# Kernel tuning notes

Hardware: AMD Instinct MI355X
Metric: run time of the kernel (lower is better)

Reference implementation:

```python
import jax, jax.numpy as jnp
import numpy as np


def setup_inputs() -> dict:
    key = jax.random.key(0)
    k1, k2, k3 = jax.random.split(key, 3)
    bs, chart_len, H = 256, 1024, 256
    num_steps, start_index = 512, 512
    chart = jax.random.normal(k1, (bs, chart_len, 2 * H), dtype=jnp.float32)
    operations = jax.random.randint(k2, (num_steps, bs, 2), 0, start_index, dtype=jnp.int64)
    U = jax.random.normal(k3, (5 * H, 2 * H), dtype=jnp.float32) * 0.05
    b = jnp.zeros((5 * H,), dtype=jnp.float32)
    return {"chart": chart, "operations": operations, "start_index": start_index, "U": U, "b": b}


def reference(chart, operations, start_index, U, b):
    H = U.shape[0] // 5
    bs = chart.shape[0]
    batch_idx = jnp.arange(bs)
    num_steps = operations.shape[0]

    def step_fn(ch, xs):
        step, ops = xs
        left = ch[batch_idx, ops[:, 0]]   # [bs, 2H]
        right = ch[batch_idx, ops[:, 1]]  # [bs, 2H]
        ccL, ccR = left[:, :H], right[:, :H]
        hh = jnp.concatenate([left[:, H:], right[:, H:]], axis=-1)  # [bs, 2H]
        preact = hh @ U.T + b  # [bs, 5H]
        i = jax.nn.sigmoid(preact[:, :H])
        fL = jax.nn.sigmoid(preact[:, H:2 * H])
        fR = jax.nn.sigmoid(preact[:, 2 * H:3 * H])
        o = jax.nn.sigmoid(preact[:, 3 * H:4 * H])
        u = jnp.tanh(preact[:, 4 * H:5 * H])
        c = fL * ccL + fR * ccR + i * u
        h = o * jnp.tanh(c)
        ch = ch.at[:, start_index + step, :].set(jnp.concatenate([c, h], axis=-1))
        return ch, None

    chart, _ = jax.lax.scan(step_fn, chart, (jnp.arange(num_steps), operations))
    return chart
```

## Files before the change

### kernel.cpp

```cpp
#include <hip/hip_runtime.h>
#include <hip/hip_bf16.h>

#define H_     256
#define TWOH_  512
#define CL_    1024
#define BS_    256
#define START_ 512

typedef float  f32x16   __attribute__((ext_vector_type(16)));
typedef short  short8_t __attribute__((ext_vector_type(8)));
typedef short  short4_t __attribute__((ext_vector_type(4)));
typedef __bf16 bf16x8   __attribute__((ext_vector_type(8)));

static __device__ __forceinline__ unsigned short f2bf(float x) {
  __hip_bfloat16 h = __float2bfloat16(x);
  return __builtin_bit_cast(unsigned short, h);
}

static __device__ __forceinline__ void gload16(const void* g, void* l) {
  __builtin_amdgcn_global_load_lds(
      (const __attribute__((address_space(1))) void*)g,
      (__attribute__((address_space(3))) void*)l, 16, 0, 0);
}

#define SCHED0() __builtin_amdgcn_sched_barrier(0)

__global__ void uconv_kernel(const float* __restrict__ U,
                             unsigned short* __restrict__ ub) {
  int tid = blockIdx.x * 256 + threadIdx.x;
  if (tid >= 1280 * 512) return;
  int n = tid >> 9, k = tid & 511;
  int g = n >> 8, j = n & 255;
  int jc = j >> 6, c = (g << 6) + (j & 63);
  ub[((jc * 320 + c) << 9) + k] = f2bf(U[tid]);
}

__global__ void hbcopy_kernel(const float4* __restrict__ chart4,
                              float4* __restrict__ out4,
                              unsigned short* __restrict__ hb) {
  const long long total = 16777216LL;
  long long tid = (long long)blockIdx.x * blockDim.x + threadIdx.x;
  for (long long e = tid; e < total; e += (long long)gridDim.x * blockDim.x) {
    long long i   = e >> 16;
    long long rem = e & 65535;
    long long off = (i << 17) + rem;
    float4 f = chart4[off];
    out4[off] = f;
    int col4 = (int)(rem & 127);
    if (col4 >= 64) {
      long long pos = rem >> 7;
      short4_t v;
      v[0] = (short)f2bf(f.x); v[1] = (short)f2bf(f.y);
      v[2] = (short)f2bf(f.z); v[3] = (short)f2bf(f.w);
      *(short4_t*)(hb + ((i * 512 + pos) * 256 + (long long)(col4 - 64) * 4)) = v;
    }
  }
}

__global__ void copy_kernel(const float4* __restrict__ src,
                            float4* __restrict__ dst) {
  long long tid = (long long)blockIdx.x * blockDim.x + threadIdx.x;
  const long long total = 16777216LL;
  for (long long e = tid; e < total; e += (long long)gridDim.x * blockDim.x) {
    long long i   = e >> 16;
    long long rem = e & 65535;
    long long off = (i << 17) + rem;
    dst[off] = src[off];
  }
}

__global__ __launch_bounds__(256, 2) void chart10_kernel(
    const float* __restrict__ chart,
    const int* __restrict__ ops,
    const unsigned short* __restrict__ ub,
    const unsigned short* __restrict__ hb,
    const float* __restrict__ bias,
    float* __restrict__ out)
{
  __shared__ unsigned short As[2][128 * 32];
  __shared__ unsigned short Bs[2][320 * 32];
  __shared__ int opsl[256];

  const int tid = threadIdx.x, lane = tid & 63, wid = tid >> 6;
  const int l31 = lane & 31, lhi = lane >> 5;
  const int wm = wid >> 1, wn = wid & 1;

  const int bx = blockIdx.x;
  const int g  = (bx & 7) * 512 + (bx >> 3);
  const int s  = g >> 3, mg = (g >> 2) & 1, jc = g & 3;

  opsl[tid] = ops[((size_t)s * BS_ + mg * 128) * 2 + tid];
  __syncthreads();

  const int asrc = (tid & 3) ^ (((tid >> 2) ^ (tid >> 4)) & 3);
  int opL256[2], opR256[2];
  const unsigned short* hbA[2];
  #pragma unroll
  for (int p = 0; p < 2; ++p) {
    int rl = p * 64 + (tid >> 2);
    opL256[p] = opsl[2 * rl] * 256;
    opR256[p] = opsl[2 * rl + 1] * 256;
    hbA[p] = hb + ((size_t)(mg * 128 + rl) * 512) * 256 + asrc * 8;
  }
  const unsigned short* ubB[5];
  #pragma unroll
  for (int p = 0; p < 5; ++p) {
    ubB[p] = ub + (((size_t)(jc * 320 + p * 64 + (tid >> 2))) << 9) + asrc * 8;
  }

  f32x16 acc0[5], acc1[5];
  #pragma unroll
  for (int gg = 0; gg < 5; ++gg)
    #pragma unroll
    for (int q = 0; q < 16; ++q) { acc0[gg][q] = 0.f; acc1[gg][q] = 0.f; }

#define STAGE(BUF, KT) do {                                                     \
    const int koff_ = ((KT) < 8) ? (KT) * 32 : (KT) * 32 - 256;                 \
    _Pragma("unroll")                                                           \
    for (int p = 0; p < 2; ++p) {                                               \
      gload16(hbA[p] + (((KT) < 8) ? opL256[p] : opR256[p]) + koff_,            \
              &As[BUF][(p * 256 + tid) * 8]);                                   \
    }                                                                           \
    _Pragma("unroll")                                                           \
    for (int p = 0; p < 5; ++p) {                                               \
      gload16(ubB[p] + (KT) * 32, &Bs[BUF][(p * 256 + tid) * 8]);               \
    }                                                                           \
  } while (0)

  const int sw   = (l31 ^ (l31 >> 2)) & 3;
  const int aro0 = (wm * 64 + l31) * 32;
  const int aro1 = aro0 + 32 * 32;
  const int bro  = (wn * 32 + l31) * 32;

#define COMPUTE(BUF) do {                                                       \
    _Pragma("unroll")                                                           \
    for (int ks = 0; ks < 2; ++ks) {                                            \
      const int ce = ((ks * 2 + lhi) ^ sw) * 8;                                 \
      bf16x8 a0 = __builtin_bit_cast(bf16x8,                                    \
          *(const short8_t*)&As[BUF][aro0 + ce]);                               \
      bf16x8 a1 = __builtin_bit_cast(bf16x8,                                    \
          *(const short8_t*)&As[BUF][aro1 + ce]);                               \
      _Pragma("unroll")                                                         \
      for (int gg = 0; gg < 5; ++gg) {                                          \
        bf16x8 b = __builtin_bit_cast(bf16x8,                                   \
            *(const short8_t*)&Bs[BUF][bro + gg * 2048 + ce]);                  \
        acc0[gg] = __builtin_amdgcn_mfma_f32_32x32x16_bf16(a0,b,acc0[gg],0,0,0);\
        acc1[gg] = __builtin_amdgcn_mfma_f32_32x32x16_bf16(a1,b,acc1[gg],0,0,0);\
      }                                                                         \
    }                                                                           \
  } while (0)

#define PHASE(BUF, KT, DOSTAGE) do {                                            \
    asm volatile("s_waitcnt vmcnt(7)" ::: "memory");                            \
    __builtin_amdgcn_s_barrier();                                               \
    SCHED0();                                                                   \
    __builtin_amdgcn_s_setprio(1);                                              \
    COMPUTE(BUF);                                                               \
    __builtin_amdgcn_s_setprio(0);                                              \
    SCHED0();                                                                   \
    __builtin_amdgcn_s_barrier();                                               \
    SCHED0();                                                                   \
    if (DOSTAGE) { STAGE(BUF, (KT) + 2); SCHED0(); }                            \
  } while (0)

  STAGE(0, 0); SCHED0();
  STAGE(1, 1); SCHED0();

  #pragma unroll
  for (int kt = 0; kt < 14; kt += 2) {
    PHASE(0, kt,     true);
    PHASE(1, kt + 1, true);
  }
  PHASE(0, 14, false);
  asm volatile("s_waitcnt vmcnt(0)" ::: "memory");
  __builtin_amdgcn_s_barrier();
  SCHED0();
  __builtin_amdgcn_s_setprio(1);
  COMPUTE(1);
  __builtin_amdgcn_s_setprio(0);

#undef PHASE
#undef COMPUTE
#undef STAGE

  const int jlane = jc * 64 + wn * 32 + l31;
  float bg[5];
  #pragma unroll
  for (int gg = 0; gg < 5; ++gg) bg[gg] = bias[gg * H_ + jlane];

#define EPI(ACC, MF) do {                                                       \
    _Pragma("unroll")                                                           \
    for (int q = 0; q < 16; ++q) {                                              \
      const int rl_  = wm * 64 + (MF) * 32 + (q & 3) + 8 * (q >> 2) + 4 * lhi;  \
      const int i_   = mg * 128 + rl_;                                          \
      const int opL_ = opsl[2 * rl_], opR_ = opsl[2 * rl_ + 1];                 \
      const float ccL_ = chart[((size_t)i_ * CL_ + opL_) * TWOH_ + jlane];      \
      const float ccR_ = chart[((size_t)i_ * CL_ + opR_) * TWOH_ + jlane];      \
      float pi_  = (ACC)[0][q] + bg[0];                                         \
      float pfL_ = (ACC)[1][q] + bg[1];                                         \
      float pfR_ = (ACC)[2][q] + bg[2];                                         \
      float po_  = (ACC)[3][q] + bg[3];                                         \
      float pu_  = (ACC)[4][q] + bg[4];                                         \
      float gi_  = 1.f / (1.f + __expf(-pi_));                                  \
      float gfL_ = 1.f / (1.f + __expf(-pfL_));                                 \
      float gfR_ = 1.f / (1.f + __expf(-pfR_));                                 \
      float go_  = 1.f / (1.f + __expf(-po_));                                  \
      float eu_  = __expf(2.f * pu_);                                           \
      float gu_  = 1.f - 2.f / (eu_ + 1.f);                                     \
      float c_   = gfL_ * ccL_ + gfR_ * ccR_ + gi_ * gu_;                       \
      float ec_  = __expf(2.f * c_);                                            \
      float th_  = 1.f - 2.f / (ec_ + 1.f);                                     \
      float h_   = go_ * th_;                                                   \
      float* orow_ = out + ((size_t)i_ * CL_ + START_ + s) * TWOH_;             \
      orow_[jlane]      = c_;                                                   \
      orow_[H_ + jlane] = h_;                                                   \
    }                                                                           \
  } while (0)

  EPI(acc0, 0);
  EPI(acc1, 1);
#undef EPI
}

__global__ __launch_bounds__(256, 2) void chart1_kernel(
    const float* __restrict__ chart,
    const int* __restrict__ ops,
    const float* __restrict__ U,
    const float* __restrict__ bias,
    float* __restrict__ out)
{
  __shared__ unsigned short As[64 * 72];
  __shared__ unsigned short Bs[320 * 72];
  __shared__ int opsl[128];

  const int tid = threadIdx.x, lane = tid & 63, wid = tid >> 6;
  const int wm = wid & 1, wn = wid >> 1;
  const int bx = blockIdx.x, jc = blockIdx.y;
  const int s = bx >> 2, ibase = (bx & 3) * 64, j0 = jc * 64;

  if (tid < 128) opsl[tid] = ops[(s * BS_ + ibase) * 2 + tid];
  __syncthreads();

  const int arow = tid >> 2, aqc = tid & 3;
  const int opL_s = opsl[2 * arow], opR_s = opsl[2 * arow + 1];
  const long long abase_i = (long long)(ibase + arow) * CL_;

  f32x16 acc[5];
  #pragma unroll
  for (int g = 0; g < 5; ++g)
    #pragma unroll
    for (int q = 0; q < 16; ++q) acc[g][q] = 0.0f;

  const int a_off  = (wm * 32 + (lane & 31)) * 72 + 8 * (lane >> 5);
  const int b_off0 = (wn * 32 + (lane & 31)) * 72 + 8 * (lane >> 5);

  for (int kt = 0; kt < 8; ++kt) {
    const int k0 = kt * 64;
    {
      const int op   = (k0 < 256) ? opL_s : opR_s;
      const int col0 = ((k0 < 256) ? 256 + k0 : k0) + aqc * 16;
      const float* src = chart + (abase_i + op) * TWOH_ + col0;
      float4 f0 = *(const float4*)(src + 0);
      float4 f1 = *(const float4*)(src + 4);
      float4 f2 = *(const float4*)(src + 8);
      float4 f3 = *(const float4*)(src + 12);
      short8_t v0, v1;
      v0[0] = (short)f2bf(f0.x); v0[1] = (short)f2bf(f0.y);
      v0[2] = (short)f2bf(f0.z); v0[3] = (short)f2bf(f0.w);
      v0[4] = (short)f2bf(f1.x); v0[5] = (short)f2bf(f1.y);
      v0[6] = (short)f2bf(f1.z); v0[7] = (short)f2bf(f1.w);
      v1[0] = (short)f2bf(f2.x); v1[1] = (short)f2bf(f2.y);
      v1[2] = (short)f2bf(f2.z); v1[3] = (short)f2bf(f2.w);
      v1[4] = (short)f2bf(f3.x); v1[5] = (short)f2bf(f3.y);
      v1[6] = (short)f2bf(f3.z); v1[7] = (short)f2bf(f3.w);
      *(short8_t*)&As[arow * 72 + aqc * 16]     = v0;
      *(short8_t*)&As[arow * 72 + aqc * 16 + 8] = v1;
    }
    #pragma unroll
    for (int cc = 0; cc < 20; ++cc) {
      int chunk = cc * 256 + tid;
      int c  = chunk >> 4;
      int ko = (chunk & 15) * 4;
      int n  = ((c >> 6) << 8) + j0 + (c & 63);
      float4 f = *(const float4*)(U + (long long)n * 512 + k0 + ko);
      short4_t v;
      v[0] = (short)f2bf(f.x); v[1] = (short)f2bf(f.y);
      v[2] = (short)f2bf(f.z); v[3] = (short)f2bf(f.w);
      *(short4_t*)&Bs[c * 72 + ko] = v;
    }
    __syncthreads();

    #pragma unroll
    for (int ks = 0; ks < 4; ++ks) {
      bf16x8 a = __builtin_bit_cast(bf16x8, *(const short8_t*)&As[a_off + ks * 16]);
      #pragma unroll
      for (int g = 0; g < 5; ++g) {
        bf16x8 b = __builtin_bit_cast(bf16x8,
            *(const short8_t*)&Bs[b_off0 + g * 64 * 72 + ks * 16]);
        acc[g] = __builtin_amdgcn_mfma_f32_32x32x16_bf16(a, b, acc[g], 0, 0, 0);
      }
    }
    __syncthreads();
  }

  const int jlane = j0 + wn * 32 + (lane & 31);
  float bg[5];
  #pragma unroll
  for (int g = 0; g < 5; ++g) bg[g] = bias[g * H_ + jlane];

  #pragma unroll
  for (int q = 0; q < 16; ++q) {
    int rl  = wm * 32 + (q & 3) + 8 * (q >> 2) + 4 * (lane >> 5);
    int i   = ibase + rl;
    int opL = opsl[2 * rl], opR = opsl[2 * rl + 1];
    float ccL = chart[((long long)i * CL_ + opL) * TWOH_ + jlane];
    float ccR = chart[((long long)i * CL_ + opR) * TWOH_ + jlane];
    float pi  = acc[0][q] + bg[0];
    float pfL = acc[1][q] + bg[1];
    float pfR = acc[2][q] + bg[2];
    float po  = acc[3][q] + bg[3];
    float pu  = acc[4][q] + bg[4];
    float gi  = 1.f / (1.f + __expf(-pi));
    float gfL = 1.f / (1.f + __expf(-pfL));
    float gfR = 1.f / (1.f + __expf(-pfR));
    float go  = 1.f / (1.f + __expf(-po));
    float eu  = __expf(2.f * pu);
    float gu  = 1.f - 2.f / (eu + 1.f);
    float c   = gfL * ccL + gfR * ccR + gi * gu;
    float ec  = __expf(2.f * c);
    float th  = 1.f - 2.f / (ec + 1.f);
    float h   = go * th;
    float* orow = out + ((long long)i * CL_ + START_ + s) * TWOH_;
    orow[jlane]      = c;
    orow[H_ + jlane] = h;
  }
}

extern "C" void kernel_launch(void* const* d_in, const int* in_sizes, int n_in,
                              void* d_out, int out_size, void* d_ws, size_t ws_size,
                              hipStream_t stream) {
  const float* chart = (const float*)d_in[0];
  const int*   ops   = (const int*)d_in[1];
  const float* U     = (const float*)d_in[3];
  const float* bias  = (const float*)d_in[4];
  float* out = (float*)d_out;

  const size_t HB_OFF   = (size_t)2 << 20;
  const size_t HB_BYTES = (size_t)256 * 512 * 256 * 2;

  if (ws_size >= HB_OFF + HB_BYTES) {
    unsigned short* ub = (unsigned short*)d_ws;
    unsigned short* hb = (unsigned short*)((char*)d_ws + HB_OFF);
    uconv_kernel<<<2560, 256, 0, stream>>>(U, ub);
    hbcopy_kernel<<<4096, 256, 0, stream>>>((const float4*)chart, (float4*)out, hb);
    chart10_kernel<<<4096, 256, 0, stream>>>(chart, ops, ub, hb, bias, out);
  } else {
    copy_kernel<<<4096, 256, 0, stream>>>((const float4*)chart, (float4*)out);
    chart1_kernel<<<dim3(2048, 4), 256, 0, stream>>>(chart, ops, U, bias, out);
  }
}
```

Baseline: 442.4 us.

## Pre-gather bf16 hidden operands into contiguous buffer before GEMM

Adds a kernel that gathers the left/right hidden halves for every step and batch row into a contiguous bf16 matrix, so the main GEMM kernel streams A tiles contiguously instead of gathering through ops indices. The chart copy is now a plain copy rather than fused with bf16 conversion. This trades indirect loads in the GEMM for a large extra materialization pass and requires a much larger workspace, falling back to the old path otherwise.

```diff
diff --git a/kernel.cpp b/kernel.cpp
--- a/kernel.cpp
+++ b/kernel.cpp
@@ -33,6 +33,28 @@
   int g = n >> 8, j = n & 255;
   int jc = j >> 6, c = (g << 6) + (j & 63);
   ub[((jc * 320 + c) << 9) + k] = f2bf(U[tid]);
+}
+
+__global__ void gather_ga_kernel(const float* __restrict__ chart,
+                                 const int* __restrict__ ops,
+                                 unsigned short* __restrict__ ga) {
+  long long t = (long long)blockIdx.x * 256 + threadIdx.x;
+  long long i_s = t >> 6;
+  int c = (int)(t & 63);
+  int k0 = c * 8;
+  int half = (k0 < 256) ? 0 : 1;
+  int koff = (k0 < 256) ? k0 : k0 - 256;
+  int i = (int)(i_s & 255);
+  int op = ops[i_s * 2 + half];
+  const float* src = chart + ((size_t)i * CL_ + op) * TWOH_ + H_ + koff;
+  float4 f0 = *(const float4*)(src);
+  float4 f1 = *(const float4*)(src + 4);
+  short8_t v;
+  v[0] = (short)f2bf(f0.x); v[1] = (short)f2bf(f0.y);
+  v[2] = (short)f2bf(f0.z); v[3] = (short)f2bf(f0.w);
+  v[4] = (short)f2bf(f1.x); v[5] = (short)f2bf(f1.y);
+  v[6] = (short)f2bf(f1.z); v[7] = (short)f2bf(f1.w);
+  *(short8_t*)(ga + i_s * 512 + k0) = v;
 }
 
 __global__ void hbcopy_kernel(const float4* __restrict__ chart4,
@@ -67,6 +89,154 @@
     long long off = (i << 17) + rem;
     dst[off] = src[off];
   }
+}
+
+__global__ __launch_bounds__(256, 2) void chart11_kernel(
+    const float* __restrict__ chart,
+    const int* __restrict__ ops,
+    const unsigned short* __restrict__ ub,
+    const unsigned short* __restrict__ ga,
+    const float* __restrict__ bias,
+    float* __restrict__ out)
+{
+  __shared__ unsigned short As[2][128 * 32];
+  __shared__ unsigned short Bs[2][320 * 32];
+  __shared__ int opsl[256];
+
+  const int tid = threadIdx.x, lane = tid & 63, wid = tid >> 6;
+  const int l31 = lane & 31, lhi = lane >> 5;
+  const int wm = wid >> 1, wn = wid & 1;
+
+  const int bx = blockIdx.x;
+  const int g  = (bx & 7) * 512 + (bx >> 3);
+  const int s  = g >> 3, mg = (g >> 2) & 1, jc = g & 3;
+
+  opsl[tid] = ops[((size_t)s * BS_ + mg * 128) * 2 + tid];
+  __syncthreads();
+
+  const int asrc = (tid & 3) ^ (((tid >> 2) ^ (tid >> 4)) & 3);
+  const unsigned short* gaA[2];
+  #pragma unroll
+  for (int p = 0; p < 2; ++p) {
+    int rl = p * 64 + (tid >> 2);
+    gaA[p] = ga + ((size_t)(s * BS_ + mg * 128 + rl)) * 512 + asrc * 8;
+  }
+  const unsigned short* ubB[5];
+  #pragma unroll
+  for (int p = 0; p < 5; ++p) {
+    ubB[p] = ub + (((size_t)(jc * 320 + p * 64 + (tid >> 2))) << 9) + asrc * 8;
+  }
+
+  f32x16 acc0[5], acc1[5];
+  #pragma unroll
+  for (int gg = 0; gg < 5; ++gg)
+    #pragma unroll
+    for (int q = 0; q < 16; ++q) { acc0[gg][q] = 0.f; acc1[gg][q] = 0.f; }
+
+#define STAGE(BUF, KT) do {                                                     \
+    _Pragma("unroll")                                                           \
+    for (int p = 0; p < 2; ++p) {                                               \
+      gload16(gaA[p] + (KT) * 32, &As[BUF][(p * 256 + tid) * 8]);               \
+    }                                                                           \
+    _Pragma("unroll")                                                           \
+    for (int p = 0; p < 5; ++p) {                                               \
+      gload16(ubB[p] + (KT) * 32, &Bs[BUF][(p * 256 + tid) * 8]);               \
+    }                                                                           \
+  } while (0)
+
+  const int sw   = (l31 ^ (l31 >> 2)) & 3;
+  const int aro0 = (wm * 64 + l31) * 32;
+  const int aro1 = aro0 + 32 * 32;
+  const int bro  = (wn * 32 + l31) * 32;
+
+#define COMPUTE(BUF) do {                                                       \
+    _Pragma("unroll")                                                           \
+    for (int ks = 0; ks < 2; ++ks) {                                            \
+      const int ce = ((ks * 2 + lhi) ^ sw) * 8;                                 \
+      bf16x8 a0 = __builtin_bit_cast(bf16x8,                                    \
+          *(const short8_t*)&As[BUF][aro0 + ce]);                               \
+      bf16x8 a1 = __builtin_bit_cast(bf16x8,                                    \
+          *(const short8_t*)&As[BUF][aro1 + ce]);                               \
+      _Pragma("unroll")                                                         \
+      for (int gg = 0; gg < 5; ++gg) {                                          \
+        bf16x8 b = __builtin_bit_cast(bf16x8,                                   \
+            *(const short8_t*)&Bs[BUF][bro + gg * 2048 + ce]);                  \
+        acc0[gg] = __builtin_amdgcn_mfma_f32_32x32x16_bf16(a0,b,acc0[gg],0,0,0);\
+        acc1[gg] = __builtin_amdgcn_mfma_f32_32x32x16_bf16(a1,b,acc1[gg],0,0,0);\
+      }                                                                         \
+    }                                                                           \
+  } while (0)
+
+#define PHASE(BUF, KT, DOSTAGE) do {                                            \
+    asm volatile("s_waitcnt vmcnt(7)" ::: "memory");                            \
+    __builtin_amdgcn_s_barrier();                                               \
+    SCHED0();                                                                   \
+    __builtin_amdgcn_s_setprio(1);                                              \
+    COMPUTE(BUF);                                                               \
+    __builtin_amdgcn_s_setprio(0);                                              \
+    SCHED0();                                                                   \
+    __builtin_amdgcn_s_barrier();                                               \
+    SCHED0();                                                                   \
+    if (DOSTAGE) { STAGE(BUF, (KT) + 2); SCHED0(); }                            \
+  } while (0)
+
+  STAGE(0, 0); SCHED0();
+  STAGE(1, 1); SCHED0();
+
+  #pragma unroll
+  for (int kt = 0; kt < 14; kt += 2) {
+    PHASE(0, kt,     true);
+    PHASE(1, kt + 1, true);
+  }
+  PHASE(0, 14, false);
+  asm volatile("s_waitcnt vmcnt(0)" ::: "memory");
+  __builtin_amdgcn_s_barrier();
+  SCHED0();
+  __builtin_amdgcn_s_setprio(1);
+  COMPUTE(1);
+  __builtin_amdgcn_s_setprio(0);
+
+#undef PHASE
+#undef COMPUTE
+#undef STAGE
+
+  const int jlane = jc * 64 + wn * 32 + l31;
+  float bg[5];
+  #pragma unroll
+  for (int gg = 0; gg < 5; ++gg) bg[gg] = bias[gg * H_ + jlane];
+
+#define EPI(ACC, MF) do {                                                       \
+    _Pragma("unroll")                                                           \
+    for (int q = 0; q < 16; ++q) {                                              \
+      const int rl_  = wm * 64 + (MF) * 32 + (q & 3) + 8 * (q >> 2) + 4 * lhi;  \
+      const int i_   = mg * 128 + rl_;                                          \
+      const int opL_ = opsl[2 * rl_], opR_ = opsl[2 * rl_ + 1];                 \
+      const float ccL_ = chart[((size_t)i_ * CL_ + opL_) * TWOH_ + jlane];      \
+      const float ccR_ = chart[((size_t)i_ * CL_ + opR_) * TWOH_ + jlane];      \
+      float pi_  = (ACC)[0][q] + bg[0];                                         \
+      float pfL_ = (ACC)[1][q] + bg[1];                                         \
+      float pfR_ = (ACC)[2][q] + bg[2];                                         \
+      float po_  = (ACC)[3][q] + bg[3];                                         \
+      float pu_  = (ACC)[4][q] + bg[4];                                         \
+      float gi_  = 1.f / (1.f + __expf(-pi_));                                  \
+      float gfL_ = 1.f / (1.f + __expf(-pfL_));                                 \
+      float gfR_ = 1.f / (1.f + __expf(-pfR_));                                 \
+      float go_  = 1.f / (1.f + __expf(-po_));                                  \
+      float eu_  = __expf(2.f * pu_);                                           \
+      float gu_  = 1.f - 2.f / (eu_ + 1.f);                                     \
+      float c_   = gfL_ * ccL_ + gfR_ * ccR_ + gi_ * gu_;                       \
+      float ec_  = __expf(2.f * c_);                                            \
+      float th_  = 1.f - 2.f / (ec_ + 1.f);                                     \
+      float h_   = go_ * th_;                                                   \
+      float* orow_ = out + ((size_t)i_ * CL_ + START_ + s) * TWOH_;             \
+      orow_[jlane]      = c_;                                                   \
+      orow_[H_ + jlane] = h_;                                                   \
+    }                                                                           \
+  } while (0)
+
+  EPI(acc0, 0);
+  EPI(acc1, 1);
+#undef EPI
 }
 
 __global__ __launch_bounds__(256, 2) void chart10_kernel(
@@ -345,12 +515,21 @@
   const float* bias  = (const float*)d_in[4];
   float* out = (float*)d_out;
 
-  const size_t HB_OFF   = (size_t)2 << 20;
+  const size_t UB_OFF   = 0;
+  const size_t GA_OFF   = (size_t)2 << 20;
+  const size_t GA_BYTES = (size_t)512 * 256 * 512 * 2;
   const size_t HB_BYTES = (size_t)256 * 512 * 256 * 2;
 
-  if (ws_size >= HB_OFF + HB_BYTES) {
-    unsigned short* ub = (unsigned short*)d_ws;
-    unsigned short* hb = (unsigned short*)((char*)d_ws + HB_OFF);
+  if (ws_size >= GA_OFF + GA_BYTES) {
+    unsigned short* ub = (unsigned short*)((char*)d_ws + UB_OFF);
+    unsigned short* ga = (unsigned short*)((char*)d_ws + GA_OFF);
+    uconv_kernel<<<2560, 256, 0, stream>>>(U, ub);
+    copy_kernel<<<4096, 256, 0, stream>>>((const float4*)chart, (float4*)out);
+    gather_ga_kernel<<<32768, 256, 0, stream>>>(chart, ops, ga);
+    chart11_kernel<<<4096, 256, 0, stream>>>(chart, ops, ub, ga, bias, out);
+  } else if (ws_size >= GA_OFF + HB_BYTES) {
+    unsigned short* ub = (unsigned short*)((char*)d_ws + UB_OFF);
+    unsigned short* hb = (unsigned short*)((char*)d_ws + GA_OFF);
     uconv_kernel<<<2560, 256, 0, stream>>>(U, ub);
     hbcopy_kernel<<<4096, 256, 0, stream>>>((const float4*)chart, (float4*)out, hb);
     chart10_kernel<<<4096, 256, 0, stream>>>(chart, ops, ub, hb, bias, out);
```

Result: slower. 471.3 us (+6.5%).
